# Kernel optimization log

Hardware: AMD Instinct MI355X
Metric: run time of the kernel (lower is better)

Reference implementation:

```python
import jax, jax.numpy as jnp
import numpy as np

K = 3  # kernel_size
P = 1  # padding


def setup_inputs() -> dict:
    key = jax.random.key(0)
    k1, k2, k3 = jax.random.split(key, 3)
    B, Cin, H, W = 4, 64, 64, 64
    Cout = 64
    L = K * K + 1  # patch length + constant-1 term = 10
    x = jax.random.normal(k1, (B, Cin, H, W), dtype=jnp.float32)
    # kaiming_uniform-like scale for filters / biases
    filters = jax.random.normal(k2, (Cout, Cin, L, L), dtype=jnp.float32) * 0.05
    biases = jax.random.normal(k3, (Cout, 1), dtype=jnp.float32) * 0.05
    return {"x": x, "filters": filters, "biases": biases}


def reference(x, filters, biases):
    # x: [B, Cin, H, W]; filters: [Cout, Cin, L, L]; biases: [Cout, 1]
    B, C, H, W = x.shape
    xp = jnp.pad(x, ((0, 0), (0, 0), (P, P), (P, P)))
    # im2col: flattened KxK patch per pixel, row-major over (dy, dx) -> [B, C, K*K, H, W]
    patches = jnp.stack(
        [xp[:, :, dy:dy + H, dx:dx + W] for dy in range(K) for dx in range(K)],
        axis=2,
    )
    # prepend constant 1 -> s: [B, C, L, H, W], L = K*K + 1
    ones = jnp.ones((B, C, 1, H, W), dtype=x.dtype)
    s = jnp.concatenate([ones, patches], axis=2)
    # per-pixel, per-channel outer product s s^T: [B, C, L, L, H, W]
    outer = s[:, :, :, None, :, :] * s[:, :, None, :, :, :]
    # quadratic-form contraction with filters, summed over (c, i, j)
    out = jnp.einsum('bcijhw,ocij->bohw', outer, filters)
    out = out + biases[:, 0][None, :, None, None]
    return out
```

## Files before the change

### kernel.cpp

```cpp
#include <hip/hip_runtime.h>
#include <hip/hip_bf16.h>


typedef __attribute__((ext_vector_type(8))) short short8;
typedef __attribute__((ext_vector_type(16))) float f32x16;

#define NCH  64
#define NOUT 64

__device__ constexpr signed char TI[56] = {
  0,0,0,0,0,0,0,0,0,
  1,2,3,4,5,6,7,8,9,
  1,1,1,1,1,1,1,1,
  2,2,2,2,2,2,2,
  3,3,3,3,3,3,
  4,4,4,4,4,
  5,5,5,5,
  6,6,6,
  7,7,
  8,
  0,0};
__device__ constexpr signed char TJ[56] = {
  1,2,3,4,5,6,7,8,9,
  1,2,3,4,5,6,7,8,9,
  2,3,4,5,6,7,8,9,
  3,4,5,6,7,8,9,
  4,5,6,7,8,9,
  5,6,7,8,9,
  6,7,8,9,
  7,8,9,
  8,9,
  9,
  0,0};

__device__ __forceinline__ unsigned short f2bf(float f) {
  __hip_bfloat16 h = __float2bfloat16(f);
  unsigned short u;
  __builtin_memcpy(&u, &h, 2);
  return u;
}

__global__ __launch_bounds__(256) void prep_w2(const float* __restrict__ F,
                                               const float* __restrict__ biases,
                                               unsigned short* __restrict__ W2) {
  int idx = blockIdx.x * 256 + threadIdx.x;
  int e = idx & 7, o = (idx >> 3) & 63;
  int rest = idx >> 9;
  int hf = rest & 1, stp = rest >> 1;
  int st = stp % 7, pair = stp / 7;
  int ch = (st < 4) ? (2 * pair + hf) : (2 * pair + 1 - hf);
  int kl = (st < 4) ? (16 * st + e) : (16 * (st - 4) + 8 + e);
  const float* base = F + (size_t)(o * NCH + ch) * 100;
  float w;
  if (kl < 54) {
    int i = TI[kl], j = TJ[kl];
    if (i == 0)      w = base[j] + base[j * 10];
    else if (i == j) w = base[i * 10 + j];
    else             w = base[i * 10 + j] + base[j * 10 + i];
  } else if (kl == 54) {
    w = base[0] + (ch == 0 ? biases[o] : 0.f);
  } else {
    w = 0.f;
  }
  W2[idx] = f2bf(w);
}

__global__ __launch_bounds__(512, 2) void poly2d_mfma(
    const float* __restrict__ x, const unsigned short* __restrict__ W2,
    float* __restrict__ out) {
  const int b = blockIdx.x >> 6, h = blockIdx.x & 63;
  const int tid = threadIdx.x;
  const int lane = tid & 63, wave = tid >> 6;
  const int px = lane & 31, hf = lane >> 5;

  __shared__ float smem[34816];

  {
    const int r = lane >> 4, q = lane & 15;
    const size_t xbase = ((size_t)b * NCH + wave * 8) * 4096;
    #pragma unroll
    for (int i = 0; i < 8; ++i) {
      float* ch0 = &smem[(wave * 8 + i) * 216];
      if (lane < 48) {
        int hh = h + r - 1;
        bool ok = (unsigned)hh < 64u;
        int hcl = ok ? hh : 0;
        float4 v = *(const float4*)&x[xbase + (size_t)i * 4096 + hcl * 64 + (q << 2)];
        if (!ok) v = make_float4(0.f, 0.f, 0.f, 0.f);
        *(float4*)&ch0[r * 72 + 4 + (q << 2)] = v;
      } else if (lane < 54) {
        int rr = (lane - 48) >> 1, side = lane & 1;
        *(float4*)&ch0[rr * 72 + (side ? 68 : 0)] = make_float4(0.f, 0.f, 0.f, 0.f);
      }
    }
  }

  f32x16 a00, a01, a10, a11;
  #pragma unroll
  for (int r = 0; r < 16; ++r) { a00[r] = 0.f; a01[r] = 0.f; a10[r] = 0.f; a11[r] = 0.f; }

  for (int stage = 0; stage < 4; ++stage) {
    const int cA = stage * 2 + hf;
    const int cB = cA ^ 1;
    const float* rA = &smem[(wave * 8 + cA) * 216 + px];
    const float* rB = &smem[(wave * 8 + cB) * 216 + px];
    float sA0[9], sA1[9], sB0[9], sB1[9];
    #pragma unroll
    for (int r = 0; r < 3; ++r) {
      #pragma unroll
      for (int d = 0; d < 3; ++d) {
        sA0[r * 3 + d] = rA[r * 72 + 3 + d];
        sA1[r * 3 + d] = rA[r * 72 + 35 + d];
        sB0[r * 3 + d] = rB[r * 72 + 3 + d];
        sB1[r * 3 + d] = rB[r * 72 + 35 + d];
      }
    }
    short8 P0[7], P1[7];
    #pragma unroll
    for (int g = 0; g < 7; ++g) {
      short8 p0, p1;
      #pragma unroll
      for (int e = 0; e < 8; ++e) {
        const int kl = (g < 4) ? (16 * g + e) : (16 * (g - 4) + 8 + e);
        const float* s0 = (g < 4) ? sA0 : sB0;
        const float* s1 = (g < 4) ? sA1 : sB1;
        float v0, v1;
        if (kl == 55)      { v0 = 0.f;   v1 = 0.f; }
        else if (kl == 54) { v0 = 1.f;   v1 = 1.f; }
        else if (kl < 9)   { v0 = s0[kl];           v1 = s1[kl]; }
        else if (kl < 18)  { float t0 = s0[kl - 9], t1 = s1[kl - 9];
                             v0 = t0 * t0;          v1 = t1 * t1; }
        else               { v0 = s0[TI[kl] - 1] * s0[TJ[kl] - 1];
                             v1 = s1[TI[kl] - 1] * s1[TJ[kl] - 1]; }
        p0[e] = (short)f2bf(v0);
        p1[e] = (short)f2bf(v1);
      }
      P0[g] = p0; P1[g] = p1;
    }
    const unsigned short* wb =
        W2 + (size_t)(wave * 4 + stage) * 7168 + hf * 512 + px * 8;
    #pragma unroll
    for (int st = 0; st < 7; ++st) {
      const short8 w0 = *(const short8*)(wb + st * 1024);
      const short8 w1 = *(const short8*)(wb + st * 1024 + 256);
      a00 = __builtin_amdgcn_mfma_f32_32x32x16_bf16(w0, P0[st], a00, 0, 0, 0);
      a10 = __builtin_amdgcn_mfma_f32_32x32x16_bf16(w1, P0[st], a10, 0, 0, 0);
      a01 = __builtin_amdgcn_mfma_f32_32x32x16_bf16(w0, P1[st], a01, 0, 0, 0);
      a11 = __builtin_amdgcn_mfma_f32_32x32x16_bf16(w1, P1[st], a11, 0, 0, 0);
    }
  }

  __syncthreads();
  {
    float* base0 = &smem[(wave * 64 + px) * 68];
    float* base1 = &smem[(wave * 64 + px + 32) * 68];
    #pragma unroll
    for (int blk = 0; blk < 4; ++blk) {
      int ob = blk * 8 + 4 * hf;
      *(float4*)&base0[ob]      = make_float4(a00[blk*4], a00[blk*4+1], a00[blk*4+2], a00[blk*4+3]);
      *(float4*)&base0[ob + 32] = make_float4(a10[blk*4], a10[blk*4+1], a10[blk*4+2], a10[blk*4+3]);
      *(float4*)&base1[ob]      = make_float4(a01[blk*4], a01[blk*4+1], a01[blk*4+2], a01[blk*4+3]);
      *(float4*)&base1[ob + 32] = make_float4(a11[blk*4], a11[blk*4+1], a11[blk*4+2], a11[blk*4+3]);
    }
  }
  __syncthreads();
  {
    const int op = wave * 8;
    float s8[8] = {0.f, 0.f, 0.f, 0.f, 0.f, 0.f, 0.f, 0.f};
    #pragma unroll
    for (int g = 0; g < 8; ++g) {
      const float* rg = &smem[(g * 64 + lane) * 68 + op];
      float4 u0 = *(const float4*)&rg[0];
      float4 u1 = *(const float4*)&rg[4];
      s8[0] += u0.x; s8[1] += u0.y; s8[2] += u0.z; s8[3] += u0.w;
      s8[4] += u1.x; s8[5] += u1.y; s8[6] += u1.z; s8[7] += u1.w;
    }
    const size_t obase = (((size_t)b * NOUT + op) * 64 + h) * 64 + lane;
    #pragma unroll
    for (int k = 0; k < 8; ++k)
      out[obase + (size_t)k * 4096] = s8[k];
  }
}

extern "C" void kernel_launch(void* const* d_in, const int* in_sizes, int n_in,
                              void* d_out, int out_size, void* d_ws, size_t ws_size,
                              hipStream_t stream) {
  const float* x       = (const float*)d_in[0];
  const float* filters = (const float*)d_in[1];
  const float* biases  = (const float*)d_in[2];
  float* out = (float*)d_out;
  unsigned short* W2 = (unsigned short*)d_ws;

  hipLaunchKernelGGL(prep_w2, dim3(896), dim3(256), 0, stream,
                     filters, biases, W2);
  hipLaunchKernelGGL(poly2d_mfma, dim3(256), dim3(512), 0, stream,
                     x, W2, out);
}
```

Before: 21.63 us.

## Stage filters in LDS for weight prep and prefetch MFMA weights per stage

```diff
diff --git a/kernel.cpp b/kernel.cpp
--- a/kernel.cpp
+++ b/kernel.cpp
@@ -43,26 +43,39 @@
 __global__ __launch_bounds__(256) void prep_w2(const float* __restrict__ F,
                                                const float* __restrict__ biases,
                                                unsigned short* __restrict__ W2) {
-  int idx = blockIdx.x * 256 + threadIdx.x;
-  int e = idx & 7, o = (idx >> 3) & 63;
-  int rest = idx >> 9;
-  int hf = rest & 1, stp = rest >> 1;
-  int st = stp % 7, pair = stp / 7;
-  int ch = (st < 4) ? (2 * pair + hf) : (2 * pair + 1 - hf);
-  int kl = (st < 4) ? (16 * st + e) : (16 * (st - 4) + 8 + e);
-  const float* base = F + (size_t)(o * NCH + ch) * 100;
-  float w;
-  if (kl < 54) {
-    int i = TI[kl], j = TJ[kl];
-    if (i == 0)      w = base[j] + base[j * 10];
-    else if (i == j) w = base[i * 10 + j];
-    else             w = base[i * 10 + j] + base[j * 10 + i];
-  } else if (kl == 54) {
-    w = base[0] + (ch == 0 ? biases[o] : 0.f);
-  } else {
-    w = 0.f;
-  }
-  W2[idx] = f2bf(w);
+  const int pair = blockIdx.x;
+  __shared__ float Fl[64 * 200];
+  __shared__ float bl[64];
+  for (int t = threadIdx.x; t < 3200; t += 256) {
+    int o = t / 50, r = t % 50;
+    *(float4*)&Fl[o * 200 + r * 4] =
+        *(const float4*)&F[((size_t)o * NCH + 2 * pair) * 100 + r * 4];
+  }
+  if (threadIdx.x < 64) bl[threadIdx.x] = biases[threadIdx.x];
+  __syncthreads();
+  for (int s = threadIdx.x; s < 896; s += 256) {
+    int o = s & 63, hf = (s >> 6) & 1, st = s >> 7;
+    int chl = (st < 4) ? hf : 1 - hf;
+    const float* base = &Fl[o * 200 + chl * 100];
+    short8 v;
+    #pragma unroll
+    for (int e = 0; e < 8; ++e) {
+      int kl = (st < 4) ? (16 * st + e) : (16 * (st - 4) + 8 + e);
+      float w;
+      if (kl < 54) {
+        int i = TI[kl], j = TJ[kl];
+        if (i == 0)      w = base[j] + base[j * 10];
+        else if (i == j) w = base[i * 10 + j];
+        else             w = base[i * 10 + j] + base[j * 10 + i];
+      } else if (kl == 54) {
+        w = base[0] + ((pair == 0 && chl == 0) ? bl[o] : 0.f);
+      } else {
+        w = 0.f;
+      }
+      v[e] = (short)f2bf(w);
+    }
+    *(short8*)&W2[(size_t)pair * 7168 + (size_t)s * 8] = v;
+  }
 }
 
 __global__ __launch_bounds__(512, 2) void poly2d_mfma(
@@ -99,9 +112,20 @@
   #pragma unroll
   for (int r = 0; r < 16; ++r) { a00[r] = 0.f; a01[r] = 0.f; a10[r] = 0.f; a11[r] = 0.f; }
 
+  #pragma unroll
   for (int stage = 0; stage < 4; ++stage) {
     const int cA = stage * 2 + hf;
     const int cB = cA ^ 1;
+
+    const unsigned short* wb =
+        W2 + (size_t)(wave * 4 + stage) * 7168 + hf * 512 + px * 8;
+    short8 w0[7], w1[7];
+    #pragma unroll
+    for (int st = 0; st < 7; ++st) {
+      w0[st] = *(const short8*)(wb + st * 1024);
+      w1[st] = *(const short8*)(wb + st * 1024 + 256);
+    }
+
     const float* rA = &smem[(wave * 8 + cA) * 216 + px];
     const float* rB = &smem[(wave * 8 + cB) * 216 + px];
     float sA0[9], sA1[9], sB0[9], sB1[9];
@@ -115,38 +139,42 @@
         sB1[r * 3 + d] = rB[r * 72 + 35 + d];
       }
     }
-    short8 P0[7], P1[7];
-    #pragma unroll
-    for (int g = 0; g < 7; ++g) {
-      short8 p0, p1;
+
+    #pragma unroll
+    for (int half = 0; half < 2; ++half) {
+      const float* sa = half ? sA1 : sA0;
+      const float* sb = half ? sB1 : sB0;
+      short8 P[7];
       #pragma unroll
-      for (int e = 0; e < 8; ++e) {
-        const int kl = (g < 4) ? (16 * g + e) : (16 * (g - 4) + 8 + e);
-        const float* s0 = (g < 4) ? sA0 : sB0;
-        const float* s1 = (g < 4) ? sA1 : sB1;
-        float v0, v1;
-        if (kl == 55)      { v0 = 0.f;   v1 = 0.f; }
-        else if (kl == 54) { v0 = 1.f;   v1 = 1.f; }
-        else if (kl < 9)   { v0 = s0[kl];           v1 = s1[kl]; }
-        else if (kl < 18)  { float t0 = s0[kl - 9], t1 = s1[kl - 9];
-                             v0 = t0 * t0;          v1 = t1 * t1; }
-        else               { v0 = s0[TI[kl] - 1] * s0[TJ[kl] - 1];
-                             v1 = s1[TI[kl] - 1] * s1[TJ[kl] - 1]; }
-        p0[e] = (short)f2bf(v0);
-        p1[e] = (short)f2bf(v1);
-      }
-      P0[g] = p0; P1[g] = p1;
-    }
-    const unsigned short* wb =
-        W2 + (size_t)(wave * 4 + stage) * 7168 + hf * 512 + px * 8;
-    #pragma unroll
-    for (int st = 0; st < 7; ++st) {
-      const short8 w0 = *(const short8*)(wb + st * 1024);
-      const short8 w1 = *(const short8*)(wb + st * 1024 + 256);
-      a00 = __builtin_amdgcn_mfma_f32_32x32x16_bf16(w0, P0[st], a00, 0, 0, 0);
-      a10 = __builtin_amdgcn_mfma_f32_32x32x16_bf16(w1, P0[st], a10, 0, 0, 0);
-      a01 = __builtin_amdgcn_mfma_f32_32x32x16_bf16(w0, P1[st], a01, 0, 0, 0);
-      a11 = __builtin_amdgcn_mfma_f32_32x32x16_bf16(w1, P1[st], a11, 0, 0, 0);
+      for (int g = 0; g < 7; ++g) {
+        short8 pk;
+        #pragma unroll
+        for (int e = 0; e < 8; ++e) {
+          const int kl = (g < 4) ? (16 * g + e) : (16 * (g - 4) + 8 + e);
+          const float* s = (g < 4) ? sa : sb;
+          float v;
+          if (kl == 55)      v = 0.f;
+          else if (kl == 54) v = 1.f;
+          else if (kl < 9)   v = s[kl];
+          else if (kl < 18)  { float t = s[kl - 9]; v = t * t; }
+          else               v = s[TI[kl] - 1] * s[TJ[kl] - 1];
+          pk[e] = (short)f2bf(v);
+        }
+        P[g] = pk;
+      }
+      if (half == 0) {
+        #pragma unroll
+        for (int st = 0; st < 7; ++st) {
+          a00 = __builtin_amdgcn_mfma_f32_32x32x16_bf16(w0[st], P[st], a00, 0, 0, 0);
+          a10 = __builtin_amdgcn_mfma_f32_32x32x16_bf16(w1[st], P[st], a10, 0, 0, 0);
+        }
+      } else {
+        #pragma unroll
+        for (int st = 0; st < 7; ++st) {
+          a01 = __builtin_amdgcn_mfma_f32_32x32x16_bf16(w0[st], P[st], a01, 0, 0, 0);
+          a11 = __builtin_amdgcn_mfma_f32_32x32x16_bf16(w1[st], P[st], a11, 0, 0, 0);
+        }
+      }
     }
   }
 
@@ -191,7 +219,7 @@
   float* out = (float*)d_out;
   unsigned short* W2 = (unsigned short*)d_ws;
 
-  hipLaunchKernelGGL(prep_w2, dim3(896), dim3(256), 0, stream,
+  hipLaunchKernelGGL(prep_w2, dim3(32), dim3(256), 0, stream,
                      filters, biases, W2);
   hipLaunchKernelGGL(poly2d_mfma, dim3(256), dim3(512), 0, stream,
                      x, W2, out);
```

After: 27.25 us. +26.0%, slower.
